# Kernel optimization log

Measured on AMD Instinct MI355X. Metric: run time of the kernel, lower is better.

The kernel has to match this reference:

```python
import jax, jax.numpy as jnp
import numpy as np

H, D, K, FF = 4, 256, 1024, 1024  # n_head, d_model, key_feature_dim, dim_feedforward
L, B = 2048, 4                    # pixels, batch


def setup_inputs() -> dict:
    key = jax.random.key(0)
    ks = jax.random.split(key, 12)
    def g(k, shape, s=0.02):
        return jax.random.normal(k, shape, jnp.float32) * s
    return dict(
        src=jax.random.normal(ks[0], (L, B, D), jnp.float32),
        WK=g(ks[1], (H, K, D), (2.0 / K) ** 0.5),
        WQ=g(ks[2], (H, K, D), (2.0 / K) ** 0.5),
        WV=g(ks[3], (H, D, D), (2.0 / D) ** 0.5),
        TC=g(ks[4], (H, D, D)),
        ENw1=g(ks[5], (H, FF, D)), ENb1=jnp.zeros((H, FF), jnp.float32),
        ENw2=g(ks[6], (H, D, FF)), ENb2=jnp.zeros((H, D), jnp.float32),
        ENg=jnp.ones((H, D), jnp.float32), ENbeta=jnp.zeros((H, D), jnp.float32),
        Wout=g(ks[7], (D, H * D)),
        L1w=g(ks[8], (FF, D)), L1b=jnp.zeros((FF,), jnp.float32),
        L2w=g(ks[9], (D, FF)), L2b=jnp.zeros((D,), jnp.float32),
        N1g=jnp.ones((D,), jnp.float32), N1b=jnp.zeros((D,), jnp.float32),
        N2g=jnp.ones((D,), jnp.float32), N2b=jnp.zeros((D,), jnp.float32),
    )


def _ln(x, g, b, eps=1e-5):
    m = jnp.mean(x, -1, keepdims=True)
    v = jnp.mean((x - m) ** 2, -1, keepdims=True)
    return (x - m) * jax.lax.rsqrt(v + eps) * g + b


def _l2n(x, eps=1e-12):
    n = jnp.sqrt(jnp.sum(x * x, -1, keepdims=True))
    return x / jnp.maximum(n, eps)


def reference(src, WK, WQ, WV, TC, ENw1, ENb1, ENw2, ENb2, ENg, ENbeta,
              Wout, L1w, L1b, L2w, L2b, N1g, N1b, N2g, N2b):
    # --- RMA: per-head RelationUnit, vectorized over head axis h ---
    wq = _l2n(jnp.einsum('lbd,hkd->hlbk', src, WQ))   # (H,L,B,K), L2-normed
    wk = _l2n(jnp.einsum('lbd,hkd->hlbk', src, WK))
    wv = jnp.einsum('lbd,hed->hlbe', src, WV)         # (H,L,B,D)
    dot = jnp.einsum('hlbk,hmbk->hblm', wq, wk)       # (H,B,Lq,Lk)
    aff = jax.nn.softmax(dot, axis=-1)                 # softmax over keys (temp=1)
    aff = aff / (1e-9 + jnp.sum(aff, axis=2, keepdims=True))  # renorm over QUERY dim (torch dim=1)
    out = jnp.einsum('hblm,hmbe->hlbe', aff, wv)       # (H,L,B,D)
    ru = jax.nn.relu(jnp.einsum('hlbe,hfe->hlbf', src[None] - out, TC))
    # per-head extra TransNonlinear: residual MLP + layernorm
    hid = jax.nn.relu(jnp.einsum('hlbd,hfd->hlbf', ru, ENw1) + ENb1[:, None, None, :])
    s2 = jnp.einsum('hlbf,hdf->hlbd', hid, ENw2) + ENb2[:, None, None, :]
    tn = _ln(ru + s2, ENg[:, None, None, :], ENbeta[:, None, None, :])  # (H,L,B,D)
    concat = jnp.transpose(tn, (1, 2, 0, 3)).reshape(L, B, H * D)
    attn = concat @ Wout.T                              # (L,B,D)
    # --- encoder layer: residual + LN + FFN + LN (dropout = eval identity) ---
    x = _ln(src + attn, N1g, N1b)
    ff = jax.nn.relu(x @ L1w.T + L1b) @ L2w.T + L2b
    return _ln(x + ff, N2g, N2b)
```

## Files before the change

kernel.cpp:

```cpp
#include <hip/hip_runtime.h>
#include <hip/hip_bf16.h>

typedef __hip_bfloat16 bf16;
typedef short s16x8 __attribute__((ext_vector_type(8)));
typedef float f32x4 __attribute__((ext_vector_type(4)));

#ifndef __has_builtin
#define __has_builtin(x) 0
#endif
#if __has_builtin(__builtin_amdgcn_global_load_lds)
#define HAS_GLL 1
#else
#define HAS_GLL 0
#endif

#define HN 4
#define DM 256
#define KF 1024
#define FFD 1024
#define LL 2048
#define BB 4
#define NN (LL * BB)
#define HD (HN * DM)

__device__ __forceinline__ float b2f(unsigned short u) {
    unsigned v = ((unsigned)u) << 16; float f; __builtin_memcpy(&f, &v, 4); return f;
}
__device__ __forceinline__ unsigned short f2b(float f) {
    bf16 b = (bf16)f; unsigned short u; __builtin_memcpy(&u, &b, 2); return u;
}

__device__ __forceinline__ float waveReduceSum(float v) {
    for (int o = 32; o; o >>= 1) v += __shfl_down(v, o, 64);
    return v;
}
__device__ __forceinline__ float waveReduceMax(float v) {
    for (int o = 32; o; o >>= 1) v = fmaxf(v, __shfl_down(v, o, 64));
    return v;
}
__device__ __forceinline__ float blockReduceSum(float v) {
    __shared__ float sh[4];
    v = waveReduceSum(v);
    __syncthreads();
    if ((threadIdx.x & 63) == 0) sh[threadIdx.x >> 6] = v;
    __syncthreads();
    return sh[0] + sh[1] + sh[2] + sh[3];
}
__device__ __forceinline__ float blockReduceMax(float v) {
    __shared__ float sh[4];
    v = waveReduceMax(v);
    __syncthreads();
    if ((threadIdx.x & 63) == 0) sh[threadIdx.x >> 6] = v;
    __syncthreads();
    return fmaxf(fmaxf(sh[0], sh[1]), fmaxf(sh[2], sh[3]));
}

__global__ void sentinel_kernel(float* out, float val) {
    if (threadIdx.x == 0 && blockIdx.x == 0) out[0] = val;
}

#if HAS_GLL
__device__ __forceinline__ void gll16(void* g, void* l) {
    __builtin_amdgcn_global_load_lds(
        (__attribute__((address_space(1))) unsigned int*)g,
        (__attribute__((address_space(3))) unsigned int*)l, 16, 0, 0);
}
#endif

__global__ __launch_bounds__(256) void gemm_nt(
    const void* __restrict__ A, int aF32, int lda, long sA,
    const void* __restrict__ Bv, int bF32, int ldb, long sB,
    void* __restrict__ C, int cF32, int ldc, long sC,
    int Kc,
    const float* __restrict__ bias, long sBias,
    const void* __restrict__ aux, int auxType, int ldaux, long sAux,
    float accSign, int relu)
{
    const int z = blockIdx.z;
    const float* Af = (const float*)A + (long)z * sA;
    const bf16*  Ah = (const bf16*)A + (long)z * sA;
    const float* Bf = (const float*)Bv + (long)z * sB;
    const bf16*  Bh = (const bf16*)Bv + (long)z * sB;
    float* Cf = (float*)C + (long)z * sC;
    bf16*  Ch = (bf16*)C + (long)z * sC;
    const float* biasp = bias ? (bias + (long)z * sBias) : nullptr;
    const float* auxf = (auxType == 1) ? ((const float*)aux + (long)z * sAux) : nullptr;
    const bf16*  auxh = (auxType == 2) ? ((const bf16*)aux + (long)z * sAux) : nullptr;

    __shared__ __align__(16) bf16 As[128 * 32];
    __shared__ __align__(16) bf16 Bs[128 * 32];

    const int tid = threadIdx.x;
    const int lane = tid & 63;
    const int wv = __builtin_amdgcn_readfirstlane(tid >> 6);
    const int wm = (tid >> 6) & 1;
    const int wn = (tid >> 6) >> 1;
    const int lrow = lane & 15;
    const int quad = lane >> 4;
    const int m0 = blockIdx.x * 128;
    const int n0 = blockIdx.y * 128;
    const int srow = tid >> 1;
    const int scol = (tid & 1) * 16;
    const int drow = wv * 16 + (lane >> 2);
    const int dcol = (lane & 3) * 8;

    f32x4 acc[4][4] = {};

    for (int k0 = 0; k0 < Kc; k0 += 32) {
        uint4 av0, av1, bv0, bv1;
        if (aF32) {
            const float* ag = Af + (long)(m0 + srow) * lda + k0 + scol;
            ushort t[16];
#pragma unroll
            for (int j = 0; j < 4; j++) {
                float4 f = *(const float4*)(ag + 4 * j);
                t[4*j] = f2b(f.x); t[4*j+1] = f2b(f.y); t[4*j+2] = f2b(f.z); t[4*j+3] = f2b(f.w);
            }
            av0 = *(const uint4*)&t[0]; av1 = *(const uint4*)&t[8];
        }
#if !HAS_GLL
        else {
            const bf16* ag = Ah + (long)(m0 + srow) * lda + k0 + scol;
            av0 = *(const uint4*)ag; av1 = *(const uint4*)(ag + 8);
        }
#endif
        if (bF32) {
            const float* bg = Bf + (long)(n0 + srow) * ldb + k0 + scol;
            ushort t[16];
#pragma unroll
            for (int j = 0; j < 4; j++) {
                float4 f = *(const float4*)(bg + 4 * j);
                t[4*j] = f2b(f.x); t[4*j+1] = f2b(f.y); t[4*j+2] = f2b(f.z); t[4*j+3] = f2b(f.w);
            }
            bv0 = *(const uint4*)&t[0]; bv1 = *(const uint4*)&t[8];
        }
#if !HAS_GLL
        else {
            const bf16* bg = Bh + (long)(n0 + srow) * ldb + k0 + scol;
            bv0 = *(const uint4*)bg; bv1 = *(const uint4*)(bg + 8);
        }
#endif
        __syncthreads();
        if (aF32) {
            *(uint4*)&As[srow * 32 + scol] = av0;
            *(uint4*)&As[srow * 32 + scol + 8] = av1;
        } else {
#if HAS_GLL
            gll16((void*)(Ah + (long)(m0 + drow) * lda + k0 + dcol), (void*)(As + wv * 512));
            gll16((void*)(Ah + (long)(m0 + 64 + drow) * lda + k0 + dcol), (void*)(As + 2048 + wv * 512));
#else
            *(uint4*)&As[srow * 32 + scol] = av0;
            *(uint4*)&As[srow * 32 + scol + 8] = av1;
#endif
        }
        if (bF32) {
            *(uint4*)&Bs[srow * 32 + scol] = bv0;
            *(uint4*)&Bs[srow * 32 + scol + 8] = bv1;
        } else {
#if HAS_GLL
            gll16((void*)(Bh + (long)(n0 + drow) * ldb + k0 + dcol), (void*)(Bs + wv * 512));
            gll16((void*)(Bh + (long)(n0 + 64 + drow) * ldb + k0 + dcol), (void*)(Bs + 2048 + wv * 512));
#else
            *(uint4*)&Bs[srow * 32 + scol] = bv0;
            *(uint4*)&Bs[srow * 32 + scol + 8] = bv1;
#endif
        }
        __syncthreads();

        s16x8 af[4], bfg[4];
#pragma unroll
        for (int mi = 0; mi < 4; mi++) {
            int r = wm * 64 + mi * 16 + lrow;
            af[mi] = *(const s16x8*)&As[r * 32 + quad * 8];
        }
#pragma unroll
        for (int ni = 0; ni < 4; ni++) {
            int r = wn * 64 + ni * 16 + lrow;
            bfg[ni] = *(const s16x8*)&Bs[r * 32 + quad * 8];
        }
#pragma unroll
        for (int mi = 0; mi < 4; mi++)
#pragma unroll
            for (int ni = 0; ni < 4; ni++)
                acc[mi][ni] = __builtin_amdgcn_mfma_f32_16x16x32_bf16(af[mi], bfg[ni], acc[mi][ni], 0, 0, 0);
    }

#pragma unroll
    for (int mi = 0; mi < 4; mi++) {
#pragma unroll
        for (int ni = 0; ni < 4; ni++) {
            int col = n0 + wn * 64 + ni * 16 + lrow;
            float bv = biasp ? biasp[col] : 0.0f;
#pragma unroll
            for (int i = 0; i < 4; i++) {
                int row = m0 + wm * 64 + mi * 16 + quad * 4 + i;
                float v = accSign * acc[mi][ni][i] + bv;
                if (auxType == 1) v += auxf[(long)row * ldaux + col];
                else if (auxType == 2) v += (float)auxh[(long)row * ldaux + col];
                if (relu) v = fmaxf(v, 0.0f);
                if (cF32) Cf[(long)row * ldc + col] = v;
                else Ch[(long)row * ldc + col] = (bf16)v;
            }
        }
    }
}

__global__ __launch_bounds__(256) void cvt4(const float* __restrict__ in, bf16* __restrict__ out, int n4) {
    int i = blockIdx.x * 256 + threadIdx.x;
    if (i < n4) {
        float4 f = ((const float4*)in)[i];
        ushort4 u; u.x = f2b(f.x); u.y = f2b(f.y); u.z = f2b(f.z); u.w = f2b(f.w);
        ((ushort4*)out)[i] = u;
    }
}

struct WCvt {
    const float* in[9];
    bf16* out[9];
    int n4[9];
};
__global__ __launch_bounds__(256) void cvt_weights(WCvt wc) {
    int t = blockIdx.y;
    int n4 = wc.n4[t];
    const float4* in = (const float4*)wc.in[t];
    ushort4* out = (ushort4*)wc.out[t];
    for (int i = blockIdx.x * 256 + threadIdx.x; i < n4; i += gridDim.x * 256) {
        float4 f = in[i];
        ushort4 u; u.x = f2b(f.x); u.y = f2b(f.y); u.z = f2b(f.z); u.w = f2b(f.w);
        out[i] = u;
    }
}

__global__ __launch_bounds__(256) void l2norm_rows(bf16* __restrict__ Q) {
    bf16* q = Q + (long)blockIdx.x * KF;
    ushort4 u = ((ushort4*)q)[threadIdx.x];
    float v0 = b2f(u.x), v1 = b2f(u.y), v2 = b2f(u.z), v3 = b2f(u.w);
    float ss = blockReduceSum(v0 * v0 + v1 * v1 + v2 * v2 + v3 * v3);
    float inv = 1.0f / fmaxf(sqrtf(ss), 1e-12f);
    u.x = f2b(v0 * inv); u.y = f2b(v1 * inv); u.z = f2b(v2 * inv); u.w = f2b(v3 * inv);
    ((ushort4*)q)[threadIdx.x] = u;
}

__global__ __launch_bounds__(256) void softmax_rows(bf16* __restrict__ P) {
    bf16* p = P + (long)blockIdx.x * LL;
    ushort4 a = ((ushort4*)p)[2 * threadIdx.x];
    ushort4 b = ((ushort4*)p)[2 * threadIdx.x + 1];
    float v[8] = {b2f(a.x), b2f(a.y), b2f(a.z), b2f(a.w), b2f(b.x), b2f(b.y), b2f(b.z), b2f(b.w)};
    float mx = -1e30f;
#pragma unroll
    for (int i = 0; i < 8; i++) mx = fmaxf(mx, v[i]);
    mx = blockReduceMax(mx);
    float s = 0.0f;
#pragma unroll
    for (int i = 0; i < 8; i++) { v[i] = __expf(v[i] - mx); s += v[i]; }
    s = blockReduceSum(s);
    float inv = 1.0f / s;
    a.x = f2b(v[0]*inv); a.y = f2b(v[1]*inv); a.z = f2b(v[2]*inv); a.w = f2b(v[3]*inv);
    b.x = f2b(v[4]*inv); b.y = f2b(v[5]*inv); b.z = f2b(v[6]*inv); b.w = f2b(v[7]*inv);
    ((ushort4*)p)[2 * threadIdx.x] = a;
    ((ushort4*)p)[2 * threadIdx.x + 1] = b;
}

__global__ __launch_bounds__(256) void zero_cs(float* __restrict__ cs) {
    cs[blockIdx.x * 256 + threadIdx.x] = 0.0f;
}

__global__ __launch_bounds__(256) void colsum2(const bf16* __restrict__ P, float* __restrict__ cs) {
    int col = blockIdx.x * 256 + threadIdx.x;
    int rc = blockIdx.y;
    int b = blockIdx.z;
    const bf16* p = P + (long)b * LL * LL + (long)rc * 128 * LL + col;
    float s = 0.0f;
#pragma unroll 4
    for (int r = 0; r < 128; r++) s += (float)p[(long)r * LL];
    atomicAdd(&cs[(long)b * LL + col], s);
}

__global__ __launch_bounds__(256) void scale_vt(bf16* __restrict__ vt, const float* __restrict__ cs) {
    int e = blockIdx.x, b = blockIdx.y;
    bf16* row = vt + ((long)b * DM + e) * LL;
    const float* c = cs + (long)b * LL;
#pragma unroll
    for (int i = 0; i < 8; i++) {
        int m = threadIdx.x + i * 256;
        row[m] = (bf16)((float)row[m] / (1e-9f + c[m]));
    }
}

__global__ __launch_bounds__(256) void ln_rows(const bf16* __restrict__ in, void* __restrict__ out,
                                               int outF32,
                                               const float* __restrict__ g, const float* __restrict__ b,
                                               const float* __restrict__ aux) {
    long base = (long)blockIdx.x * 256;
    float v = (float)in[base + threadIdx.x];
    if (aux) v += aux[base + threadIdx.x];
    float mean = blockReduceSum(v) * (1.0f / 256.0f);
    float d = v - mean;
    float var = blockReduceSum(d * d) * (1.0f / 256.0f);
    float o = d * rsqrtf(var + 1e-5f) * g[threadIdx.x] + b[threadIdx.x];
    if (outF32) ((float*)out)[base + threadIdx.x] = o;
    else ((bf16*)out)[base + threadIdx.x] = (bf16)o;
}

__global__ __launch_bounds__(256) void ln_cat(bf16* __restrict__ cat, const float* __restrict__ g,
                                              const float* __restrict__ bb) {
    long n = blockIdx.x;
    int h = blockIdx.y;
    bf16* x = cat + n * HD + (long)h * DM;
    float v = (float)x[threadIdx.x];
    float mean = blockReduceSum(v) * (1.0f / 256.0f);
    float d = v - mean;
    float var = blockReduceSum(d * d) * (1.0f / 256.0f);
    x[threadIdx.x] = (bf16)(d * rsqrtf(var + 1e-5f) * g[h * DM + threadIdx.x] + bb[h * DM + threadIdx.x]);
}

extern "C" void kernel_launch(void* const* d_in, const int* in_sizes, int n_in,
                              void* d_out, int out_size, void* d_ws, size_t ws_size,
                              hipStream_t stream) {
    const float* src  = (const float*)d_in[0];
    const float* WK   = (const float*)d_in[1];
    const float* WQ   = (const float*)d_in[2];
    const float* WV   = (const float*)d_in[3];
    const float* TC   = (const float*)d_in[4];
    const float* ENw1 = (const float*)d_in[5];
    const float* ENb1 = (const float*)d_in[6];
    const float* ENw2 = (const float*)d_in[7];
    const float* ENb2 = (const float*)d_in[8];
    const float* ENg  = (const float*)d_in[9];
    const float* ENbt = (const float*)d_in[10];
    const float* Wout = (const float*)d_in[11];
    const float* L1w  = (const float*)d_in[12];
    const float* L1b  = (const float*)d_in[13];
    const float* L2w  = (const float*)d_in[14];
    const float* L2b  = (const float*)d_in[15];
    const float* N1g  = (const float*)d_in[16];
    const float* N1b  = (const float*)d_in[17];
    const float* N2g  = (const float*)d_in[18];
    const float* N2b  = (const float*)d_in[19];

    const size_t COMPACT_FLOOR = 34700000;
    const size_t FAST_FLOOR  = 92307456;
    const size_t FASTW_FLOOR = 92307456 + 11010048;
    if (ws_size < COMPACT_FLOOR || out_size != NN * DM || n_in != 20) {
        float val;
        if (n_in != 20) val = 32768.0f + (float)n_in;
        else if (out_size != NN * DM) val = 49152.0f;
        else val = 16384.0f + 128.0f * (float)(unsigned)(ws_size >> 20);
        sentinel_kernel<<<1, 64, 0, stream>>>((float*)d_out, val);
        return;
    }

    char* w = (char*)d_ws;
    auto G = [&](const void* A, int aF, int lda, long sA,
                 const void* B, int bF, int ldb, long sB,
                 void* C, int cF, int ldc, long sC,
                 int M, int Nn, int Kc, int nb,
                 const float* bias, long sBias,
                 const void* aux, int auxT, int ldaux, long sAux,
                 float sgn, int relu) {
        gemm_nt<<<dim3(M / 128, Nn / 128, nb), dim3(256), 0, stream>>>(
            A, aF, lda, sA, B, bF, ldb, sB, C, cF, ldc, sC, Kc,
            bias, sBias, aux, auxT, ldaux, sAux, sgn, relu);
    };

    if (ws_size >= FAST_FLOOR) {
        bf16*  Sb  = (bf16*)(w + 0);
        bf16*  Q   = (bf16*)(w + 4194304);
        bf16*  K   = (bf16*)(w + 20971520);
        bf16*  Vt  = (bf16*)(w + 37748736);
        bf16*  P   = (bf16*)(w + 41943040);
        bf16*  Su  = (bf16*)(w + 75497472);
        float* Cs  = (float*)(w + 92274688);
        bf16* Ru = Q; bf16* Hid = K; bf16* Cat = P;
        bf16* Attn = Vt; bf16* Xln = Su; bf16* Ffh = Q; bf16* Yp = Vt;

        const int haveWb = (ws_size >= FASTW_FLOOR) ? 1 : 0;
        char* wb = w + 92307456;
        bf16* WKb   = (bf16*)(wb + 0);
        bf16* WQb   = (bf16*)(wb + 2097152);
        bf16* WVb   = (bf16*)(wb + 4194304);
        bf16* TCb   = (bf16*)(wb + 4718592);
        bf16* ENw1b = (bf16*)(wb + 5242880);
        bf16* ENw2b = (bf16*)(wb + 7340032);
        bf16* Woutb = (bf16*)(wb + 9437184);
        bf16* L1wb  = (bf16*)(wb + 9961472);
        bf16* L2wb  = (bf16*)(wb + 10485760);
        if (haveWb) {
            WCvt wc;
            wc.in[0] = WK;   wc.out[0] = WKb;   wc.n4[0] = 262144;
            wc.in[1] = WQ;   wc.out[1] = WQb;   wc.n4[1] = 262144;
            wc.in[2] = WV;   wc.out[2] = WVb;   wc.n4[2] = 65536;
            wc.in[3] = TC;   wc.out[3] = TCb;   wc.n4[3] = 65536;
            wc.in[4] = ENw1; wc.out[4] = ENw1b; wc.n4[4] = 262144;
            wc.in[5] = ENw2; wc.out[5] = ENw2b; wc.n4[5] = 262144;
            wc.in[6] = Wout; wc.out[6] = Woutb; wc.n4[6] = 65536;
            wc.in[7] = L1w;  wc.out[7] = L1wb;  wc.n4[7] = 65536;
            wc.in[8] = L2w;  wc.out[8] = L2wb;  wc.n4[8] = 65536;
            cvt_weights<<<dim3(256, 9), 256, 0, stream>>>(wc);
        }
        const int wF = haveWb ? 0 : 1;
        auto WP = [&](const void* f32p, const void* b16p, long off) {
            return haveWb ? (const void*)((const bf16*)b16p + off)
                          : (const void*)((const float*)f32p + off);
        };

        cvt4<<<2048, 256, 0, stream>>>(src, Sb, NN * DM / 4);

        for (int h = 0; h < HN; h++) {
            G(Sb, 0, DM, 0, WP(WQ, WQb, (long)h * KF * DM), wF, DM, 0, Q, 0, KF, 0,
              NN, KF, DM, 1, nullptr, 0, nullptr, 0, 0, 0, 1.0f, 0);
            G(Sb, 0, DM, 0, WP(WK, WKb, (long)h * KF * DM), wF, DM, 0, K, 0, KF, 0,
              NN, KF, DM, 1, nullptr, 0, nullptr, 0, 0, 0, 1.0f, 0);
            G(WP(WV, WVb, (long)h * DM * DM), wF, DM, 0, Sb, 0, BB * DM, DM,
              Vt, 0, LL, (long)DM * LL,
              DM, LL, DM, BB, nullptr, 0, nullptr, 0, 0, 0, 1.0f, 0);
            l2norm_rows<<<NN, 256, 0, stream>>>(Q);
            l2norm_rows<<<NN, 256, 0, stream>>>(K);
            G(Q, 0, BB * KF, KF, K, 0, BB * KF, KF, P, 0, LL, (long)LL * LL,
              LL, LL, KF, BB, nullptr, 0, nullptr, 0, 0, 0, 1.0f, 0);
            softmax_rows<<<BB * LL, 256, 0, stream>>>(P);
            zero_cs<<<BB * LL / 256, 256, 0, stream>>>(Cs);
            colsum2<<<dim3(LL / 256, 16, BB), 256, 0, stream>>>(P, Cs);
            scale_vt<<<dim3(DM, BB), 256, 0, stream>>>(Vt, Cs);
            G(P, 0, LL, (long)LL * LL, Vt, 0, LL, (long)DM * LL,
              Su + (long)h * NN * DM, 0, BB * DM, DM,
              LL, DM, LL, BB, nullptr, 0, Sb, 2, BB * DM, DM, -1.0f, 0);
        }
        G(Su, 0, DM, (long)NN * DM, WP(TC, TCb, 0), wF, DM, (long)DM * DM,
          Ru, 0, DM, (long)NN * DM,
          NN, DM, DM, HN, nullptr, 0, nullptr, 0, 0, 0, 1.0f, 1);
        for (int h = 0; h < HN; h++) {
            G(Ru + (long)h * NN * DM, 0, DM, 0, WP(ENw1, ENw1b, (long)h * FFD * DM), wF, DM, 0,
              Hid, 0, FFD, 0, NN, FFD, DM, 1, ENb1 + (long)h * FFD, 0, nullptr, 0, 0, 0, 1.0f, 1);
            G(Hid, 0, FFD, 0, WP(ENw2, ENw2b, (long)h * DM * FFD), wF, FFD, 0,
              Cat + (long)h * DM, 0, HD, 0, NN, DM, FFD, 1,
              ENb2 + (long)h * DM, 0, Ru + (long)h * NN * DM, 2, DM, 0, 1.0f, 0);
        }
        ln_cat<<<dim3(NN, HN), 256, 0, stream>>>(Cat, ENg, ENbt);
        G(Cat, 0, HD, 0, WP(Wout, Woutb, 0), wF, HD, 0, Attn, 0, DM, 0,
          NN, DM, HD, 1, nullptr, 0, nullptr, 0, 0, 0, 1.0f, 0);
        ln_rows<<<NN, 256, 0, stream>>>(Attn, Xln, 0, N1g, N1b, src);
        G(Xln, 0, DM, 0, WP(L1w, L1wb, 0), wF, DM, 0, Ffh, 0, FFD, 0,
          NN, FFD, DM, 1, L1b, 0, nullptr, 0, 0, 0, 1.0f, 1);
        G(Ffh, 0, FFD, 0, WP(L2w, L2wb, 0), wF, FFD, 0, Yp, 0, DM, 0,
          NN, DM, FFD, 1, L2b, 0, Xln, 2, DM, 0, 1.0f, 0);
        ln_rows<<<NN, 256, 0, stream>>>(Yp, (float*)d_out, 1, N2g, N2b, nullptr);
    } else {
        bf16*  S0 = (bf16*)(w + 0);
        bf16*  S1 = (bf16*)(w + 16777216);
        bf16*  S2 = (bf16*)(w + 20971520);
        bf16*  S3 = (bf16*)(w + 25165824);
        bf16*  S4 = (bf16*)(w + 26214400);
        bf16*  S5 = (bf16*)(w + 30408704);
        float* Cs = (float*)(w + 34603008);

        for (int h = 0; h < HN; h++) {
            for (int b = 0; b < BB; b++) {
                G(src + b * DM, 1, BB * DM, 0, WQ + (long)h * KF * DM, 1, DM, 0,
                  S1, 0, KF, 0, LL, KF, DM, 1, nullptr, 0, nullptr, 0, 0, 0, 1.0f, 0);
                G(src + b * DM, 1, BB * DM, 0, WK + (long)h * KF * DM, 1, DM, 0,
                  S2, 0, KF, 0, LL, KF, DM, 1, nullptr, 0, nullptr, 0, 0, 0, 1.0f, 0);
                G(WV + (long)h * DM * DM, 1, DM, 0, src + b * DM, 1, BB * DM, 0,
                  S3, 0, LL, 0, DM, LL, DM, 1, nullptr, 0, nullptr, 0, 0, 0, 1.0f, 0);
                l2norm_rows<<<LL, 256, 0, stream>>>(S1);
                l2norm_rows<<<LL, 256, 0, stream>>>(S2);
                G(S1, 0, KF, 0, S2, 0, KF, 0, S0, 0, LL, 0,
                  LL, LL, KF, 1, nullptr, 0, nullptr, 0, 0, 0, 1.0f, 0);
                softmax_rows<<<LL, 256, 0, stream>>>(S0);
                zero_cs<<<LL / 256, 256, 0, stream>>>(Cs);
                colsum2<<<dim3(LL / 256, 16, 1), 256, 0, stream>>>(S0, Cs);
                scale_vt<<<dim3(DM, 1), 256, 0, stream>>>(S3, Cs);
                G(S0, 0, LL, 0, S3, 0, LL, 0, S4 + b * DM, 0, BB * DM, 0,
                  LL, DM, LL, 1, nullptr, 0, src + b * DM, 1, BB * DM, 0, -1.0f, 0);
            }
            G(S4, 0, DM, 0, TC + (long)h * DM * DM, 1, DM, 0, S1, 0, DM, 0,
              NN, DM, DM, 1, nullptr, 0, nullptr, 0, 0, 0, 1.0f, 1);
            G(S1, 0, DM, 0, ENw1 + (long)h * FFD * DM, 1, DM, 0, S0, 0, FFD, 0,
              NN, FFD, DM, 1, ENb1 + (long)h * FFD, 0, nullptr, 0, 0, 0, 1.0f, 1);
            G(S0, 0, FFD, 0, ENw2 + (long)h * DM * FFD, 1, FFD, 0, S2, 0, DM, 0,
              NN, DM, FFD, 1, ENb2 + (long)h * DM, 0, S1, 2, DM, 0, 1.0f, 0);
            ln_rows<<<NN, 256, 0, stream>>>(S2, S2, 0, ENg + (long)h * DM, ENbt + (long)h * DM, nullptr);
            G(S2, 0, DM, 0, Wout + (long)h * DM, 1, HD, 0, S5, 0, DM, 0,
              NN, DM, DM, 1, nullptr, 0, (h == 0) ? nullptr : (const void*)S5,
              (h == 0) ? 0 : 2, DM, 0, 1.0f, 0);
        }
        ln_rows<<<NN, 256, 0, stream>>>(S5, S1, 0, N1g, N1b, src);
        G(S1, 0, DM, 0, L1w, 1, DM, 0, S0, 0, FFD, 0,
          NN, FFD, DM, 1, L1b, 0, nullptr, 0, 0, 0, 1.0f, 1);
        G(S0, 0, FFD, 0, L2w, 1, FFD, 0, S2, 0, DM, 0,
          NN, DM, FFD, 1, L2b, 0, S1, 2, DM, 0, 1.0f, 0);
        ln_rows<<<NN, 256, 0, stream>>>(S2, (float*)d_out, 1, N2g, N2b, nullptr);
    }
}
```

Before: 1.281 ms.

## Add split-K atomic GEMMs, swizzled LDS tiles, and fused Q/K projection path

Adds a split-K mode to the GEMM that accumulates partial products into fp32 outputs with atomics. It is used for the attention-times-V, Wout and L2 GEMMs, which have a small N and a long K, to raise block parallelism. The LDS tile layout gets an XOR swizzle to reduce bank conflicts on MFMA fragment reads. A new large-workspace path batches the Q and K projections into one launch and pre-initialises the residual and bias outputs with dedicated kernels. The cost is fp32 atomic traffic, extra zero and init passes, and a dependence on the workspace size reaching the new threshold.

```diff
diff --git a/kernel.cpp b/kernel.cpp
--- a/kernel.cpp
+++ b/kernel.cpp
@@ -71,21 +71,22 @@
     const void* __restrict__ A, int aF32, int lda, long sA,
     const void* __restrict__ Bv, int bF32, int ldb, long sB,
     void* __restrict__ C, int cF32, int ldc, long sC,
-    int Kc,
+    int Kc, int splitK,
     const float* __restrict__ bias, long sBias,
     const void* __restrict__ aux, int auxType, int ldaux, long sAux,
     float accSign, int relu)
 {
-    const int z = blockIdx.z;
-    const float* Af = (const float*)A + (long)z * sA;
-    const bf16*  Ah = (const bf16*)A + (long)z * sA;
-    const float* Bf = (const float*)Bv + (long)z * sB;
-    const bf16*  Bh = (const bf16*)Bv + (long)z * sB;
-    float* Cf = (float*)C + (long)z * sC;
-    bf16*  Ch = (bf16*)C + (long)z * sC;
-    const float* biasp = bias ? (bias + (long)z * sBias) : nullptr;
-    const float* auxf = (auxType == 1) ? ((const float*)aux + (long)z * sAux) : nullptr;
-    const bf16*  auxh = (auxType == 2) ? ((const bf16*)aux + (long)z * sAux) : nullptr;
+    int zb = blockIdx.z, k0base = 0, KcEff = Kc;
+    if (splitK > 1) { int chunk = zb % splitK; zb /= splitK; KcEff = Kc / splitK; k0base = chunk * KcEff; }
+    const float* Af = (const float*)A + (long)zb * sA;
+    const bf16*  Ah = (const bf16*)A + (long)zb * sA;
+    const float* Bf = (const float*)Bv + (long)zb * sB;
+    const bf16*  Bh = (const bf16*)Bv + (long)zb * sB;
+    float* Cf = (float*)C + (long)zb * sC;
+    bf16*  Ch = (bf16*)C + (long)zb * sC;
+    const float* biasp = bias ? (bias + (long)zb * sBias) : nullptr;
+    const float* auxf = (auxType == 1) ? ((const float*)aux + (long)zb * sAux) : nullptr;
+    const bf16*  auxh = (auxType == 2) ? ((const bf16*)aux + (long)zb * sAux) : nullptr;
 
     __shared__ __align__(16) bf16 As[128 * 32];
     __shared__ __align__(16) bf16 Bs[128 * 32];
@@ -101,12 +102,15 @@
     const int n0 = blockIdx.y * 128;
     const int srow = tid >> 1;
     const int scol = (tid & 1) * 16;
+    const int ssw = (srow >> 1) & 3;
+    const int c0 = scol >> 3;
     const int drow = wv * 16 + (lane >> 2);
-    const int dcol = (lane & 3) * 8;
+    const int gswc = ((lane & 3) ^ ((lane >> 3) & 3)) * 8;
+    const int aswz = (lrow >> 1) & 3;
 
     f32x4 acc[4][4] = {};
 
-    for (int k0 = 0; k0 < Kc; k0 += 32) {
+    for (int k0 = k0base; k0 < k0base + KcEff; k0 += 32) {
         uint4 av0, av1, bv0, bv1;
         if (aF32) {
             const float* ag = Af + (long)(m0 + srow) * lda + k0 + scol;
@@ -142,27 +146,27 @@
 #endif
         __syncthreads();
         if (aF32) {
-            *(uint4*)&As[srow * 32 + scol] = av0;
-            *(uint4*)&As[srow * 32 + scol + 8] = av1;
+            *(uint4*)&As[srow * 32 + ((c0 ^ ssw) * 8)] = av0;
+            *(uint4*)&As[srow * 32 + (((c0 + 1) ^ ssw) * 8)] = av1;
         } else {
 #if HAS_GLL
-            gll16((void*)(Ah + (long)(m0 + drow) * lda + k0 + dcol), (void*)(As + wv * 512));
-            gll16((void*)(Ah + (long)(m0 + 64 + drow) * lda + k0 + dcol), (void*)(As + 2048 + wv * 512));
+            gll16((void*)(Ah + (long)(m0 + drow) * lda + k0 + gswc), (void*)(As + wv * 512));
+            gll16((void*)(Ah + (long)(m0 + 64 + drow) * lda + k0 + gswc), (void*)(As + 2048 + wv * 512));
 #else
-            *(uint4*)&As[srow * 32 + scol] = av0;
-            *(uint4*)&As[srow * 32 + scol + 8] = av1;
+            *(uint4*)&As[srow * 32 + ((c0 ^ ssw) * 8)] = av0;
+            *(uint4*)&As[srow * 32 + (((c0 + 1) ^ ssw) * 8)] = av1;
 #endif
         }
         if (bF32) {
-            *(uint4*)&Bs[srow * 32 + scol] = bv0;
-            *(uint4*)&Bs[srow * 32 + scol + 8] = bv1;
+            *(uint4*)&Bs[srow * 32 + ((c0 ^ ssw) * 8)] = bv0;
+            *(uint4*)&Bs[srow * 32 + (((c0 + 1) ^ ssw) * 8)] = bv1;
         } else {
 #if HAS_GLL
-            gll16((void*)(Bh + (long)(n0 + drow) * ldb + k0 + dcol), (void*)(Bs + wv * 512));
-            gll16((void*)(Bh + (long)(n0 + 64 + drow) * ldb + k0 + dcol), (void*)(Bs + 2048 + wv * 512));
+            gll16((void*)(Bh + (long)(n0 + drow) * ldb + k0 + gswc), (void*)(Bs + wv * 512));
+            gll16((void*)(Bh + (long)(n0 + 64 + drow) * ldb + k0 + gswc), (void*)(Bs + 2048 + wv * 512));
 #else
-            *(uint4*)&Bs[srow * 32 + scol] = bv0;
-            *(uint4*)&Bs[srow * 32 + scol + 8] = bv1;
+            *(uint4*)&Bs[srow * 32 + ((c0 ^ ssw) * 8)] = bv0;
+            *(uint4*)&Bs[srow * 32 + (((c0 + 1) ^ ssw) * 8)] = bv1;
 #endif
         }
         __syncthreads();
@@ -171,12 +175,12 @@
 #pragma unroll
         for (int mi = 0; mi < 4; mi++) {
             int r = wm * 64 + mi * 16 + lrow;
-            af[mi] = *(const s16x8*)&As[r * 32 + quad * 8];
+            af[mi] = *(const s16x8*)&As[r * 32 + ((quad ^ aswz) * 8)];
         }
 #pragma unroll
         for (int ni = 0; ni < 4; ni++) {
             int r = wn * 64 + ni * 16 + lrow;
-            bfg[ni] = *(const s16x8*)&Bs[r * 32 + quad * 8];
+            bfg[ni] = *(const s16x8*)&Bs[r * 32 + ((quad ^ aswz) * 8)];
         }
 #pragma unroll
         for (int mi = 0; mi < 4; mi++)
@@ -194,12 +198,16 @@
 #pragma unroll
             for (int i = 0; i < 4; i++) {
                 int row = m0 + wm * 64 + mi * 16 + quad * 4 + i;
-                float v = accSign * acc[mi][ni][i] + bv;
-                if (auxType == 1) v += auxf[(long)row * ldaux + col];
-                else if (auxType == 2) v += (float)auxh[(long)row * ldaux + col];
-                if (relu) v = fmaxf(v, 0.0f);
-                if (cF32) Cf[(long)row * ldc + col] = v;
-                else Ch[(long)row * ldc + col] = (bf16)v;
+                if (splitK > 1) {
+                    atomicAdd(&Cf[(long)row * ldc + col], accSign * acc[mi][ni][i]);
+                } else {
+                    float v = accSign * acc[mi][ni][i] + bv;
+                    if (auxType == 1) v += auxf[(long)row * ldaux + col];
+                    else if (auxType == 2) v += (float)auxh[(long)row * ldaux + col];
+                    if (relu) v = fmaxf(v, 0.0f);
+                    if (cF32) Cf[(long)row * ldc + col] = v;
+                    else Ch[(long)row * ldc + col] = (bf16)v;
+                }
             }
         }
     }
@@ -214,11 +222,7 @@
     }
 }
 
-struct WCvt {
-    const float* in[9];
-    bf16* out[9];
-    int n4[9];
-};
+struct WCvt { const float* in[9]; bf16* out[9]; int n4[9]; };
 __global__ __launch_bounds__(256) void cvt_weights(WCvt wc) {
     int t = blockIdx.y;
     int n4 = wc.n4[t];
@@ -231,6 +235,23 @@
     }
 }
 
+__global__ __launch_bounds__(256) void su_init(const float* __restrict__ src, float* __restrict__ su) {
+    int i = blockIdx.x * 256 + threadIdx.x;
+    float4 v = ((const float4*)src)[i];
+#pragma unroll
+    for (int h = 0; h < HN; h++) ((float4*)su)[(long)h * (NN * DM / 4) + i] = v;
+}
+
+__global__ __launch_bounds__(256) void zero_f32(float* __restrict__ p) {
+    ((float4*)p)[blockIdx.x * 256 + threadIdx.x] = make_float4(0.f, 0.f, 0.f, 0.f);
+}
+
+__global__ __launch_bounds__(256) void yp_init(float* __restrict__ yp, const float* __restrict__ l2b,
+                                               const bf16* __restrict__ xln) {
+    long base = (long)blockIdx.x * DM;
+    yp[base + threadIdx.x] = l2b[threadIdx.x] + (float)xln[base + threadIdx.x];
+}
+
 __global__ __launch_bounds__(256) void l2norm_rows(bf16* __restrict__ Q) {
     bf16* q = Q + (long)blockIdx.x * KF;
     ushort4 u = ((ushort4*)q)[threadIdx.x];
@@ -287,12 +308,13 @@
     }
 }
 
-__global__ __launch_bounds__(256) void ln_rows(const bf16* __restrict__ in, void* __restrict__ out,
-                                               int outF32,
-                                               const float* __restrict__ g, const float* __restrict__ b,
-                                               const float* __restrict__ aux) {
+__global__ __launch_bounds__(256) void ln_rows2(const void* __restrict__ in, int inF32,
+                                                void* __restrict__ out, int outF32,
+                                                const float* __restrict__ g, const float* __restrict__ b,
+                                                const float* __restrict__ aux) {
     long base = (long)blockIdx.x * 256;
-    float v = (float)in[base + threadIdx.x];
+    float v = inF32 ? ((const float*)in)[base + threadIdx.x]
+                    : (float)((const bf16*)in)[base + threadIdx.x];
     if (aux) v += aux[base + threadIdx.x];
     float mean = blockReduceSum(v) * (1.0f / 256.0f);
     float d = v - mean;
@@ -341,6 +363,7 @@
     const size_t COMPACT_FLOOR = 34700000;
     const size_t FAST_FLOOR  = 92307456;
     const size_t FASTW_FLOOR = 92307456 + 11010048;
+    const size_t NEW_FLOOR   = 120094720;
     if (ws_size < COMPACT_FLOOR || out_size != NN * DM || n_in != 20) {
         float val;
         if (n_in != 20) val = 32768.0f + (float)n_in;
@@ -354,16 +377,99 @@
     auto G = [&](const void* A, int aF, int lda, long sA,
                  const void* B, int bF, int ldb, long sB,
                  void* C, int cF, int ldc, long sC,
-                 int M, int Nn, int Kc, int nb,
+                 int M, int Nn, int Kc, int nb, int splitK,
                  const float* bias, long sBias,
                  const void* aux, int auxT, int ldaux, long sAux,
                  float sgn, int relu) {
-        gemm_nt<<<dim3(M / 128, Nn / 128, nb), dim3(256), 0, stream>>>(
-            A, aF, lda, sA, B, bF, ldb, sB, C, cF, ldc, sC, Kc,
+        gemm_nt<<<dim3(M / 128, Nn / 128, nb * splitK), dim3(256), 0, stream>>>(
+            A, aF, lda, sA, B, bF, ldb, sB, C, cF, ldc, sC, Kc, splitK,
             bias, sBias, aux, auxT, ldaux, sAux, sgn, relu);
     };
 
-    if (ws_size >= FAST_FLOOR) {
+    auto setupWeights = [&](char* wb, bf16*& WQb, bf16*& WKb, bf16*& WVb, bf16*& TCb,
+                            bf16*& ENw1b, bf16*& ENw2b, bf16*& Woutb, bf16*& L1wb, bf16*& L2wb) {
+        WQb   = (bf16*)(wb + 0);
+        WKb   = (bf16*)(wb + 2097152);
+        WVb   = (bf16*)(wb + 4194304);
+        TCb   = (bf16*)(wb + 4718592);
+        ENw1b = (bf16*)(wb + 5242880);
+        ENw2b = (bf16*)(wb + 7340032);
+        Woutb = (bf16*)(wb + 9437184);
+        L1wb  = (bf16*)(wb + 9961472);
+        L2wb  = (bf16*)(wb + 10485760);
+        WCvt wc;
+        wc.in[0] = WQ;   wc.out[0] = WQb;   wc.n4[0] = 262144;
+        wc.in[1] = WK;   wc.out[1] = WKb;   wc.n4[1] = 262144;
+        wc.in[2] = WV;   wc.out[2] = WVb;   wc.n4[2] = 65536;
+        wc.in[3] = TC;   wc.out[3] = TCb;   wc.n4[3] = 65536;
+        wc.in[4] = ENw1; wc.out[4] = ENw1b; wc.n4[4] = 262144;
+        wc.in[5] = ENw2; wc.out[5] = ENw2b; wc.n4[5] = 262144;
+        wc.in[6] = Wout; wc.out[6] = Woutb; wc.n4[6] = 65536;
+        wc.in[7] = L1w;  wc.out[7] = L1wb;  wc.n4[7] = 65536;
+        wc.in[8] = L2w;  wc.out[8] = L2wb;  wc.n4[8] = 65536;
+        cvt_weights<<<dim3(256, 9), 256, 0, stream>>>(wc);
+    };
+
+    if (ws_size >= NEW_FLOOR) {
+        bf16*  Sb   = (bf16*)(w + 0);
+        bf16*  Q    = (bf16*)(w + 4194304);
+        bf16*  K    = (bf16*)(w + 20971520);
+        bf16*  Vt   = (bf16*)(w + 37748736);
+        bf16*  P    = (bf16*)(w + 41943040);
+        float* Su   = (float*)(w + 75497472);
+        float* Cs   = (float*)(w + 109051904);
+        char*  wb   = w + 109084672;
+        bf16* Ru = Q; bf16* Hid = K; bf16* Ffh = K; bf16* Cat = P;
+        float* Attn = (float*)(w + 4194304);
+        float* Yp   = (float*)(w + 12582912);
+        bf16* Xln   = (bf16*)(w + 75497472);
+
+        bf16 *WQb, *WKb, *WVb, *TCb, *ENw1b, *ENw2b, *Woutb, *L1wb, *L2wb;
+        setupWeights(wb, WQb, WKb, WVb, TCb, ENw1b, ENw2b, Woutb, L1wb, L2wb);
+        cvt4<<<2048, 256, 0, stream>>>(src, Sb, NN * DM / 4);
+        su_init<<<2048, 256, 0, stream>>>(src, Su);
+
+        for (int h = 0; h < HN; h++) {
+            G(Sb, 0, DM, 0, WQb + (long)h * KF * DM, 0, DM, 1048576,
+              Q, 0, KF, 8388608, NN, KF, DM, 2, 1,
+              nullptr, 0, nullptr, 0, 0, 0, 1.0f, 0);
+            G(WVb + (long)h * DM * DM, 0, DM, 0, Sb, 0, BB * DM, DM,
+              Vt, 0, LL, (long)DM * LL, DM, LL, DM, BB, 1,
+              nullptr, 0, nullptr, 0, 0, 0, 1.0f, 0);
+            l2norm_rows<<<2 * NN, 256, 0, stream>>>(Q);
+            G(Q, 0, BB * KF, KF, K, 0, BB * KF, KF, P, 0, LL, (long)LL * LL,
+              LL, LL, KF, BB, 1, nullptr, 0, nullptr, 0, 0, 0, 1.0f, 0);
+            softmax_rows<<<BB * LL, 256, 0, stream>>>(P);
+            zero_cs<<<BB * LL / 256, 256, 0, stream>>>(Cs);
+            colsum2<<<dim3(LL / 256, 16, BB), 256, 0, stream>>>(P, Cs);
+            scale_vt<<<dim3(DM, BB), 256, 0, stream>>>(Vt, Cs);
+            G(P, 0, LL, (long)LL * LL, Vt, 0, LL, (long)DM * LL,
+              Su + (long)h * NN * DM, 1, BB * DM, DM,
+              LL, DM, LL, BB, 4, nullptr, 0, nullptr, 0, 0, 0, -1.0f, 0);
+        }
+        G(Su, 1, DM, (long)NN * DM, TCb, 0, DM, (long)DM * DM,
+          Ru, 0, DM, (long)NN * DM, NN, DM, DM, HN, 1,
+          nullptr, 0, nullptr, 0, 0, 0, 1.0f, 1);
+        for (int h = 0; h < HN; h++) {
+            G(Ru + (long)h * NN * DM, 0, DM, 0, ENw1b + (long)h * FFD * DM, 0, DM, 0,
+              Hid, 0, FFD, 0, NN, FFD, DM, 1, 1,
+              ENb1 + (long)h * FFD, 0, nullptr, 0, 0, 0, 1.0f, 1);
+            G(Hid, 0, FFD, 0, ENw2b + (long)h * DM * FFD, 0, FFD, 0,
+              Cat + (long)h * DM, 0, HD, 0, NN, DM, FFD, 1, 1,
+              ENb2 + (long)h * DM, 0, Ru + (long)h * NN * DM, 2, DM, 0, 1.0f, 0);
+        }
+        ln_cat<<<dim3(NN, HN), 256, 0, stream>>>(Cat, ENg, ENbt);
+        zero_f32<<<NN * DM / 1024, 256, 0, stream>>>(Attn);
+        G(Cat, 0, HD, 0, Woutb, 0, HD, 0, Attn, 1, DM, 0,
+          NN, DM, HD, 1, 4, nullptr, 0, nullptr, 0, 0, 0, 1.0f, 0);
+        ln_rows2<<<NN, 256, 0, stream>>>(Attn, 1, Xln, 0, N1g, N1b, src);
+        G(Xln, 0, DM, 0, L1wb, 0, DM, 0, Ffh, 0, FFD, 0,
+          NN, FFD, DM, 1, 1, L1b, 0, nullptr, 0, 0, 0, 1.0f, 1);
+        yp_init<<<NN, 256, 0, stream>>>(Yp, L2b, Xln);
+        G(Ffh, 0, FFD, 0, L2wb, 0, FFD, 0, Yp, 1, DM, 0,
+          NN, DM, FFD, 1, 4, nullptr, 0, nullptr, 0, 0, 0, 1.0f, 0);
+        ln_rows2<<<NN, 256, 0, stream>>>(Yp, 1, (float*)d_out, 1, N2g, N2b, nullptr);
+    } else if (ws_size >= FAST_FLOOR) {
         bf16*  Sb  = (bf16*)(w + 0);
         bf16*  Q   = (bf16*)(w + 4194304);
         bf16*  K   = (bf16*)(w + 20971520);
@@ -375,29 +481,10 @@
         bf16* Attn = Vt; bf16* Xln = Su; bf16* Ffh = Q; bf16* Yp = Vt;
 
         const int haveWb = (ws_size >= FASTW_FLOOR) ? 1 : 0;
-        char* wb = w + 92307456;
-        bf16* WKb   = (bf16*)(wb + 0);
-        bf16* WQb   = (bf16*)(wb + 2097152);
-        bf16* WVb   = (bf16*)(wb + 4194304);
-        bf16* TCb   = (bf16*)(wb + 4718592);
-        bf16* ENw1b = (bf16*)(wb + 5242880);
-        bf16* ENw2b = (bf16*)(wb + 7340032);
-        bf16* Woutb = (bf16*)(wb + 9437184);
-        bf16* L1wb  = (bf16*)(wb + 9961472);
-        bf16* L2wb  = (bf16*)(wb + 10485760);
-        if (haveWb) {
-            WCvt wc;
-            wc.in[0] = WK;   wc.out[0] = WKb;   wc.n4[0] = 262144;
-            wc.in[1] = WQ;   wc.out[1] = WQb;   wc.n4[1] = 262144;
-            wc.in[2] = WV;   wc.out[2] = WVb;   wc.n4[2] = 65536;
-            wc.in[3] = TC;   wc.out[3] = TCb;   wc.n4[3] = 65536;
-            wc.in[4] = ENw1; wc.out[4] = ENw1b; wc.n4[4] = 262144;
-            wc.in[5] = ENw2; wc.out[5] = ENw2b; wc.n4[5] = 262144;
-            wc.in[6] = Wout; wc.out[6] = Woutb; wc.n4[6] = 65536;
-            wc.in[7] = L1w;  wc.out[7] = L1wb;  wc.n4[7] = 65536;
-            wc.in[8] = L2w;  wc.out[8] = L2wb;  wc.n4[8] = 65536;
-            cvt_weights<<<dim3(256, 9), 256, 0, stream>>>(wc);
-        }
+        bf16 *WQb = nullptr, *WKb = nullptr, *WVb = nullptr, *TCb = nullptr, *ENw1b = nullptr,
+             *ENw2b = nullptr, *Woutb = nullptr, *L1wb = nullptr, *L2wb = nullptr;
+        if (haveWb)
+            setupWeights(w + 92307456, WQb, WKb, WVb, TCb, ENw1b, ENw2b, Woutb, L1wb, L2wb);
         const int wF = haveWb ? 0 : 1;
         auto WP = [&](const void* f32p, const void* b16p, long off) {
             return haveWb ? (const void*)((const bf16*)b16p + off)
@@ -408,43 +495,44 @@
 
         for (int h = 0; h < HN; h++) {
             G(Sb, 0, DM, 0, WP(WQ, WQb, (long)h * KF * DM), wF, DM, 0, Q, 0, KF, 0,
-              NN, KF, DM, 1, nullptr, 0, nullptr, 0, 0, 0, 1.0f, 0);
+              NN, KF, DM, 1, 1, nullptr, 0, nullptr, 0, 0, 0, 1.0f, 0);
             G(Sb, 0, DM, 0, WP(WK, WKb, (long)h * KF * DM), wF, DM, 0, K, 0, KF, 0,
-              NN, KF, DM, 1, nullptr, 0, nullptr, 0, 0, 0, 1.0f, 0);
+              NN, KF, DM, 1, 1, nullptr, 0, nullptr, 0, 0, 0, 1.0f, 0);
             G(WP(WV, WVb, (long)h * DM * DM), wF, DM, 0, Sb, 0, BB * DM, DM,
-              Vt, 0, LL, (long)DM * LL,
-              DM, LL, DM, BB, nullptr, 0, nullptr, 0, 0, 0, 1.0f, 0);
+              Vt, 0, LL, (long)DM * LL, DM, LL, DM, BB, 1,
+              nullptr, 0, nullptr, 0, 0, 0, 1.0f, 0);
             l2norm_rows<<<NN, 256, 0, stream>>>(Q);
             l2norm_rows<<<NN, 256, 0, stream>>>(K);
             G(Q, 0, BB * KF, KF, K, 0, BB * KF, KF, P, 0, LL, (long)LL * LL,
-              LL, LL, KF, BB, nullptr, 0, nullptr, 0, 0, 0, 1.0f, 0);
+              LL, LL, KF, BB, 1, nullptr, 0, nullptr, 0, 0, 0, 1.0f, 0);
             softmax_rows<<<BB * LL, 256, 0, stream>>>(P);
             zero_cs<<<BB * LL / 256, 256, 0, stream>>>(Cs);
             colsum2<<<dim3(LL / 256, 16, BB), 256, 0, stream>>>(P, Cs);
             scale_vt<<<dim3(DM, BB), 256, 0, stream>>>(Vt, Cs);
             G(P, 0, LL, (long)LL * LL, Vt, 0, LL, (long)DM * LL,
               Su + (long)h * NN * DM, 0, BB * DM, DM,
-              LL, DM, LL, BB, nullptr, 0, Sb, 2, BB * DM, DM, -1.0f, 0);
+              LL, DM, LL, BB, 1, nullptr, 0, Sb, 2, BB * DM, DM, -1.0f, 0);
         }
         G(Su, 0, DM, (long)NN * DM, WP(TC, TCb, 0), wF, DM, (long)DM * DM,
-          Ru, 0, DM, (long)NN * DM,
-          NN, DM, DM, HN, nullptr, 0, nullptr, 0, 0, 0, 1.0f, 1);
+          Ru, 0, DM, (long)NN * DM, NN, DM, DM, HN, 1,
+          nullptr, 0, nullptr, 0, 0, 0, 1.0f, 1);
         for (int h = 0; h < HN; h++) {
             G(Ru + (long)h * NN * DM, 0, DM, 0, WP(ENw1, ENw1b, (long)h * FFD * DM), wF, DM, 0,
-              Hid, 0, FFD, 0, NN, FFD, DM, 1, ENb1 + (long)h * FFD, 0, nullptr, 0, 0, 0, 1.0f, 1);
+              Hid, 0, FFD, 0, NN, FFD, DM, 1, 1,
+              ENb1 + (long)h * FFD, 0, nullptr, 0, 0, 0, 1.0f, 1);
             G(Hid, 0, FFD, 0, WP(ENw2, ENw2b, (long)h * DM * FFD), wF, FFD, 0,
-              Cat + (long)h * DM, 0, HD, 0, NN, DM, FFD, 1,
+              Cat + (long)h * DM, 0, HD, 0, NN, DM, FFD, 1, 1,
               ENb2 + (long)h * DM, 0, Ru + (long)h * NN * DM, 2, DM, 0, 1.0f, 0);
         }
         ln_cat<<<dim3(NN, HN), 256, 0, stream>>>(Cat, ENg, ENbt);
         G(Cat, 0, HD, 0, WP(Wout, Woutb, 0), wF, HD, 0, Attn, 0, DM, 0,
-          NN, DM, HD, 1, nullptr, 0, nullptr, 0, 0, 0, 1.0f, 0);
-        ln_rows<<<NN, 256, 0, stream>>>(Attn, Xln, 0, N1g, N1b, src);
+          NN, DM, HD, 1, 1, nullptr, 0, nullptr, 0, 0, 0, 1.0f, 0);
+        ln_rows2<<<NN, 256, 0, stream>>>(Attn, 0, Xln, 0, N1g, N1b, src);
         G(Xln, 0, DM, 0, WP(L1w, L1wb, 0), wF, DM, 0, Ffh, 0, FFD, 0,
-          NN, FFD, DM, 1, L1b, 0, nullptr, 0, 0, 0, 1.0f, 1);
+          NN, FFD, DM, 1, 1, L1b, 0, nullptr, 0, 0, 0, 1.0f, 1);
         G(Ffh, 0, FFD, 0, WP(L2w, L2wb, 0), wF, FFD, 0, Yp, 0, DM, 0,
-          NN, DM, FFD, 1, L2b, 0, Xln, 2, DM, 0, 1.0f, 0);
-        ln_rows<<<NN, 256, 0, stream>>>(Yp, (float*)d_out, 1, N2g, N2b, nullptr);
+          NN, DM, FFD, 1, 1, L2b, 0, Xln, 2, DM, 0, 1.0f, 0);
+        ln_rows2<<<NN, 256, 0, stream>>>(Yp, 0, (float*)d_out, 1, N2g, N2b, nullptr);
     } else {
         bf16*  S0 = (bf16*)(w + 0);
         bf16*  S1 = (bf16*)(w + 16777216);
@@ -457,38 +545,38 @@
         for (int h = 0; h < HN; h++) {
             for (int b = 0; b < BB; b++) {
                 G(src + b * DM, 1, BB * DM, 0, WQ + (long)h * KF * DM, 1, DM, 0,
-                  S1, 0, KF, 0, LL, KF, DM, 1, nullptr, 0, nullptr, 0, 0, 0, 1.0f, 0);
+                  S1, 0, KF, 0, LL, KF, DM, 1, 1, nullptr, 0, nullptr, 0, 0, 0, 1.0f, 0);
                 G(src + b * DM, 1, BB * DM, 0, WK + (long)h * KF * DM, 1, DM, 0,
-                  S2, 0, KF, 0, LL, KF, DM, 1, nullptr, 0, nullptr, 0, 0, 0, 1.0f, 0);
+                  S2, 0, KF, 0, LL, KF, DM, 1, 1, nullptr, 0, nullptr, 0, 0, 0, 1.0f, 0);
                 G(WV + (long)h * DM * DM, 1, DM, 0, src + b * DM, 1, BB * DM, 0,
-                  S3, 0, LL, 0, DM, LL, DM, 1, nullptr, 0, nullptr, 0, 0, 0, 1.0f, 0);
+                  S3, 0, LL, 0, DM, LL, DM, 1, 1, nullptr, 0, nullptr, 0, 0, 0, 1.0f, 0);
                 l2norm_rows<<<LL, 256, 0, stream>>>(S1);
                 l2norm_rows<<<LL, 256, 0, stream>>>(S2);
                 G(S1, 0, KF, 0, S2, 0, KF, 0, S0, 0, LL, 0,
-                  LL, LL, KF, 1, nullptr, 0, nullptr, 0, 0, 0, 1.0f, 0);
+                  LL, LL, KF, 1, 1, nullptr, 0, nullptr, 0, 0, 0, 1.0f, 0);
                 softmax_rows<<<LL, 256, 0, stream>>>(S0);
                 zero_cs<<<LL / 256, 256, 0, stream>>>(Cs);
                 colsum2<<<dim3(LL / 256, 16, 1), 256, 0, stream>>>(S0, Cs);
                 scale_vt<<<dim3(DM, 1), 256, 0, stream>>>(S3, Cs);
                 G(S0, 0, LL, 0, S3, 0, LL, 0, S4 + b * DM, 0, BB * DM, 0,
-                  LL, DM, LL, 1, nullptr, 0, src + b * DM, 1, BB * DM, 0, -1.0f, 0);
+                  LL, DM, LL, 1, 1, nullptr, 0, src + b * DM, 1, BB * DM, 0, -1.0f, 0);
             }
             G(S4, 0, DM, 0, TC + (long)h * DM * DM, 1, DM, 0, S1, 0, DM, 0,
-              NN, DM, DM, 1, nullptr, 0, nullptr, 0, 0, 0, 1.0f, 1);
+              NN, DM, DM, 1, 1, nullptr, 0, nullptr, 0, 0, 0, 1.0f, 1);
             G(S1, 0, DM, 0, ENw1 + (long)h * FFD * DM, 1, DM, 0, S0, 0, FFD, 0,
-              NN, FFD, DM, 1, ENb1 + (long)h * FFD, 0, nullptr, 0, 0, 0, 1.0f, 1);
+              NN, FFD, DM, 1, 1, ENb1 + (long)h * FFD, 0, nullptr, 0, 0, 0, 1.0f, 1);
             G(S0, 0, FFD, 0, ENw2 + (long)h * DM * FFD, 1, FFD, 0, S2, 0, DM, 0,
-              NN, DM, FFD, 1, ENb2 + (long)h * DM, 0, S1, 2, DM, 0, 1.0f, 0);
-            ln_rows<<<NN, 256, 0, stream>>>(S2, S2, 0, ENg + (long)h * DM, ENbt + (long)h * DM, nullptr);
+              NN, DM, FFD, 1, 1, ENb2 + (long)h * DM, 0, S1, 2, DM, 0, 1.0f, 0);
+            ln_rows2<<<NN, 256, 0, stream>>>(S2, 0, S2, 0, ENg + (long)h * DM, ENbt + (long)h * DM, nullptr);
             G(S2, 0, DM, 0, Wout + (long)h * DM, 1, HD, 0, S5, 0, DM, 0,
-              NN, DM, DM, 1, nullptr, 0, (h == 0) ? nullptr : (const void*)S5,
+              NN, DM, DM, 1, 1, nullptr, 0, (h == 0) ? nullptr : (const void*)S5,
               (h == 0) ? 0 : 2, DM, 0, 1.0f, 0);
         }
-        ln_rows<<<NN, 256, 0, stream>>>(S5, S1, 0, N1g, N1b, src);
+        ln_rows2<<<NN, 256, 0, stream>>>(S5, 0, S1, 0, N1g, N1b, src);
         G(S1, 0, DM, 0, L1w, 1, DM, 0, S0, 0, FFD, 0,
-          NN, FFD, DM, 1, L1b, 0, nullptr, 0, 0, 0, 1.0f, 1);
+          NN, FFD, DM, 1, 1, L1b, 0, nullptr, 0, 0, 0, 1.0f, 1);
         G(S0, 0, FFD, 0, L2w, 1, FFD, 0, S2, 0, DM, 0,
-          NN, DM, FFD, 1, L2b, 0, S1, 2, DM, 0, 1.0f, 0);
-        ln_rows<<<NN, 256, 0, stream>>>(S2, (float*)d_out, 1, N2g, N2b, nullptr);
-    }
-}
+          NN, DM, FFD, 1, 1, L2b, 0, S1, 2, DM, 0, 1.0f, 0);
+        ln_rows2<<<NN, 256, 0, stream>>>(S2, 0, (float*)d_out, 1, N2g, N2b, nullptr);
+    }
+}
```

Result: slower. 1.377 ms (+7.4%).
